# Kernel optimization log

Measured on AMD Instinct MI355X. Metric: run time of the kernel, lower is better.

## Reference

```python
import jax, jax.numpy as jnp
import numpy as np

BATCH, SEQ, HEADS, EMB = 16, 4096, 16, 64
SHAPE = int(SEQ ** 0.5)          # 64 (2D grid side)
N = 2 * SHAPE - 1                # 127 (circular conv length)


def setup_inputs() -> dict:
    key = jax.random.key(0)
    k_v, k_w = jax.random.split(key)
    v = jax.random.normal(k_v, (BATCH, SEQ, HEADS, EMB), dtype=jnp.float32)
    # 'full' bias base: learned relative bias of length 2*shape_-1 per head
    w = jax.random.normal(k_w, (1, HEADS, N), dtype=jnp.float32)
    o_ = jnp.ones((SHAPE,), dtype=jnp.float32)
    return {"v": v, "w": w, "o_": o_}


def reference(v, w, o_):
    B, S, H, E = v.shape
    s = int(S ** 0.5)
    n = 2 * s - 1

    # bias_base_type == 'full': slice w[..., shape_-s : shape_+s-1] == all of w
    z_fft = jnp.fft.rfft(w)                              # (1, H, n//2+1) complex

    # v: [B, S, H, E] -> [B, E, H, s1, s2]
    vt = jnp.transpose(v, (0, 3, 2, 1)).reshape(B, E, H, s, s)
    v_s = vt.sum(axis=3)                                 # sum over s1 -> [B, E, H, s2]
    u_s = vt.sum(axis=4)                                 # sum over s2 -> [B, E, H, s1]

    pad = ((0, 0), (0, 0), (0, 0), (s - 1, 0))
    v_m_fft = jnp.fft.rfft(jnp.pad(v_s, pad))            # [B, E, H, n//2+1]
    u_m_fft = jnp.fft.rfft(jnp.pad(u_s, pad))

    zf = z_fft[:, None]                                  # (1, 1, H, n//2+1)
    RxV = jnp.fft.irfft(v_m_fft * zf, n=n)[..., :s]      # [B, E, H, s]
    RxU = jnp.fft.irfft(u_m_fft * zf, n=n)[..., :s]      # [B, E, H, s]

    # outer sum over the 2D grid, flatten back to seq
    pbv = RxV[..., None, :] + RxU[..., :, None]          # [B, E, H, s, s]
    pbv = pbv.reshape(B, E, H, S)
    pbv = jnp.transpose(pbv, (0, 3, 2, 1))               # [B, S, H, E]

    # normalizer term z_pb (batch independent)
    o_pad = jnp.pad(o_, ((s - 1, 0),))                   # (n,)
    o_fft = jnp.fft.rfft(o_pad)                          # (n//2+1,)
    z_pb = jnp.fft.irfft(o_fft * z_fft, n=n)[..., :s] * s  # (1, H, s)
    z_pb = z_pb[..., None, :] + z_pb[..., :, None]       # (1, H, s, s)
    z_pb = z_pb.reshape(-1, H, s * s)                    # (1, H, S)
    z_pb = jnp.transpose(z_pb, (0, 2, 1))                # (1, S, H)

    return pbv, z_pb
```

## Files before the change

### kernel.cpp

```cpp
#include <hip/hip_runtime.h>

#define BATCH 16
#define SEQ   4096
#define HEADS 16
#define EMB   64
#define SS    64
#define NW    127

#define RX_ELEMS (BATCH * SS * HEADS * EMB)

__global__ __launch_bounds__(256, 4) void reduce_conv_kernel(
    const float* __restrict__ v, const float* __restrict__ w,
    float* __restrict__ rxv, float* __restrict__ rxu)
{
    __shared__ float vsf[SS][SS];
    __shared__ float usl[16][SS];
    __shared__ float wtab[NW];

    const int blk  = blockIdx.x;
    const int c    = blk & 3;
    const int bh   = blk >> 2;
    const int b    = bh >> 4;
    const int h    = bh & (HEADS - 1);
    const int tid  = threadIdx.x;
    const int wave = tid >> 6;
    const int lane = tid & 63;

    for (int idx = tid; idx < SS * SS; idx += 256) (&vsf[0][0])[idx] = 0.0f;
    if (tid < NW) wtab[tid] = w[h * NW + tid];
    __syncthreads();

    const float* vbase = v + ((size_t)b * SEQ * HEADS + h) * EMB + lane;
    float vsacc[SS];
    #pragma unroll
    for (int j = 0; j < SS; ++j) vsacc[j] = 0.0f;

    const int r0 = wave * 4;
    for (int rr = 0; rr < 4; ++rr) {
        const int i = c * 16 + r0 + rr;
        const float* rowp = vbase + (size_t)i * SS * (HEADS * EMB);
        float uacc = 0.0f;
        #pragma unroll
        for (int j = 0; j < SS; ++j) {
            const float val = rowp[(size_t)j * (HEADS * EMB)];
            uacc += val;
            vsacc[j] += val;
        }
        usl[r0 + rr][lane] = uacc;
    }
    #pragma unroll
    for (int j = 0; j < SS; ++j) atomicAdd(&vsf[j][lane], vsacc[j]);
    __syncthreads();

    const int t0 = wave * 16;
    float accv[16], accu[16];
    #pragma unroll
    for (int tt = 0; tt < 16; ++tt) { accv[tt] = 0.0f; accu[tt] = 0.0f; }

    #pragma unroll
    for (int jb = 0; jb < 4; ++jb) {
        float wreg[31];
        #pragma unroll
        for (int d = 0; d < 31; ++d) {
            int idx = t0 - jb * 16 + 49 + d;
            if (idx >= NW) idx -= NW;
            wreg[d] = wtab[idx];
        }
        #pragma unroll
        for (int jj = 0; jj < 16; ++jj) {
            const float cv = vsf[jb * 16 + jj][lane];
            #pragma unroll
            for (int tt = 0; tt < 16; ++tt)
                accv[tt] += wreg[15 + tt - jj] * cv;
        }
    }
    {
        float wreg[31];
        #pragma unroll
        for (int d = 0; d < 31; ++d) {
            int idx = t0 - c * 16 + 49 + d;
            if (idx >= NW) idx -= NW;
            wreg[d] = wtab[idx];
        }
        #pragma unroll
        for (int rr = 0; rr < 16; ++rr) {
            const float cu = usl[rr][lane];
            #pragma unroll
            for (int tt = 0; tt < 16; ++tt)
                accu[tt] += wreg[15 + tt - rr] * cu;
        }
    }

    const size_t base = (((size_t)b * SS) << 10) + (h << 6) + lane;
    #pragma unroll
    for (int tt = 0; tt < 16; ++tt) {
        const size_t o = base + ((size_t)(t0 + tt) << 10);
        atomicAdd(&rxv[o], accv[tt]);
        atomicAdd(&rxu[o], accu[tt]);
    }
}

__global__ __launch_bounds__(256) void expand_kernel(
    const float* __restrict__ rxv, const float* __restrict__ rxu,
    float* __restrict__ out)
{
    const int blk = blockIdx.x;
    const int b   = blk >> 6;
    const int tid = threadIdx.x;

    const float4 ru = *((const float4*)(rxu + ((size_t)blk << 10)) + tid);
    const float4* rvb = (const float4*)(rxv + ((size_t)b << 16));
    float4* ob = (float4*)(out + (((size_t)blk) << 16)) + tid;

    #pragma unroll 8
    for (int j = 0; j < SS; ++j) {
        float4 rv = rvb[(j << 8) + tid];
        float4 r;
        r.x = rv.x + ru.x; r.y = rv.y + ru.y;
        r.z = rv.z + ru.z; r.w = rv.w + ru.w;
        ob[(size_t)j << 8] = r;
    }
}

__global__ __launch_bounds__(256) void zpb_kernel(const float* __restrict__ w,
                                                  const float* __restrict__ o_,
                                                  float* __restrict__ out2) {
    __shared__ float zp[HEADS][SS];
    __shared__ float osh[SS];
    __shared__ float wsh[HEADS * NW];

    const int tid = threadIdx.x;
    const int g   = blockIdx.x;

    if (tid < SS) osh[tid] = o_[tid];
    for (int idx = tid; idx < HEADS * NW; idx += 256) wsh[idx] = w[idx];
    __syncthreads();

    for (int idx = tid; idx < HEADS * SS; idx += 256) {
        const int h = idx / SS, t = idx % SS;
        float acc = 0.0f;
        #pragma unroll
        for (int j = 0; j < SS; ++j) {
            int k = t - j + 64;
            if (k >= NW) k -= NW;
            acc += osh[j] * wsh[h * NW + k];
        }
        zp[h][t] = acc * (float)SS;
    }
    __syncthreads();

    for (int idx = tid; idx < SS * HEADS; idx += 256) {
        const int tl = idx / HEADS, h = idx % HEADS;
        out2[(size_t)(g * SS + tl) * HEADS + h] = zp[h][tl] + zp[h][g];
    }
}

extern "C" void kernel_launch(void* const* d_in, const int* in_sizes, int n_in,
                              void* d_out, int out_size, void* d_ws, size_t ws_size,
                              hipStream_t stream) {
    const float* v  = (const float*)d_in[0];
    const float* w  = (const float*)d_in[1];
    const float* o_ = (const float*)d_in[2];
    float* out = (float*)d_out;

    float* rxv = (float*)d_ws;
    float* rxu = rxv + RX_ELEMS;

    hipMemsetAsync(d_ws, 0, (size_t)2 * RX_ELEMS * sizeof(float), stream);

    reduce_conv_kernel<<<BATCH * HEADS * 4, 256, 0, stream>>>(v, w, rxv, rxu);
    expand_kernel<<<BATCH * SS, 256, 0, stream>>>(rxv, rxu, out);

    const size_t out1_elems = (size_t)BATCH * SEQ * HEADS * EMB;
    zpb_kernel<<<SS, 256, 0, stream>>>(w, o_, out + out1_elems);
}
```

Baseline: 567.2 us.

## Split reduction and convolution into separate kernels with vectorized coalesced sums

Replaces the fused reduce+conv kernel with a sums kernel that streams v using float4 loads over the full contiguous head×emb plane (1024-thread blocks) and writes row and column sums to workspace. A second conv kernel then runs one block per (batch, head), doing both convolutions in one pass and storing with plain writes instead of atomics. The intent is better memory coalescing and bandwidth on the dominant read of v, at the cost of an extra kernel launch, an extra workspace round trip, and global atomics for the column sums.

```diff
diff --git a/kernel.cpp b/kernel.cpp
--- a/kernel.cpp
+++ b/kernel.cpp
@@ -6,50 +6,90 @@
 #define EMB   64
 #define SS    64
 #define NW    127
-
-#define RX_ELEMS (BATCH * SS * HEADS * EMB)
-
-__global__ __launch_bounds__(256, 4) void reduce_conv_kernel(
-    const float* __restrict__ v, const float* __restrict__ w,
-    float* __restrict__ rxv, float* __restrict__ rxu)
+#define PLANE (HEADS * EMB)
+
+#define SUMS_ELEMS (BATCH * SS * PLANE)
+
+__global__ __launch_bounds__(1024) void sums_kernel(
+    const float4* __restrict__ v4, float* __restrict__ vs,
+    float4* __restrict__ us4)
 {
-    __shared__ float vsf[SS][SS];
-    __shared__ float usl[16][SS];
+    __shared__ float4 upart[4][4][256];
+
+    const int blk = blockIdx.x;
+    const int b   = blk >> 4;
+    const int ic  = blk & 15;
+    const int tid = threadIdx.x;
+    const int g   = tid >> 8;
+    const int t   = tid & 255;
+
+    const float4* base = v4 + ((size_t)(b * SEQ + ic * 256) << 8) + t;
+
+    float4 uacc[4], vacc[16];
+    #pragma unroll
+    for (int il = 0; il < 4; ++il) uacc[il] = make_float4(0.f, 0.f, 0.f, 0.f);
+    #pragma unroll
+    for (int jj = 0; jj < 16; ++jj) vacc[jj] = make_float4(0.f, 0.f, 0.f, 0.f);
+
+    #pragma unroll
+    for (int il = 0; il < 4; ++il) {
+        const float4* p = base + ((size_t)(il * 64 + g * 16) << 8);
+        #pragma unroll
+        for (int jj = 0; jj < 16; ++jj) {
+            const float4 x = p[(size_t)jj << 8];
+            uacc[il].x += x.x; uacc[il].y += x.y; uacc[il].z += x.z; uacc[il].w += x.w;
+            vacc[jj].x += x.x; vacc[jj].y += x.y; vacc[jj].z += x.z; vacc[jj].w += x.w;
+        }
+    }
+
+    #pragma unroll
+    for (int il = 0; il < 4; ++il) upart[g][il][t] = uacc[il];
+    __syncthreads();
+    {
+        const int il2 = tid >> 8;
+        float4 s = upart[0][il2][t];
+        #pragma unroll
+        for (int gg = 1; gg < 4; ++gg) {
+            const float4 q = upart[gg][il2][t];
+            s.x += q.x; s.y += q.y; s.z += q.z; s.w += q.w;
+        }
+        us4[((size_t)(b * SS + ic * 4 + il2) << 8) + t] = s;
+    }
+
+    float* vsp = vs + ((size_t)(b * SS + g * 16) << 10) + (t << 2);
+    #pragma unroll
+    for (int jj = 0; jj < 16; ++jj) {
+        float* p = vsp + ((size_t)jj << 10);
+        atomicAdd(p + 0, vacc[jj].x);
+        atomicAdd(p + 1, vacc[jj].y);
+        atomicAdd(p + 2, vacc[jj].z);
+        atomicAdd(p + 3, vacc[jj].w);
+    }
+}
+
+__global__ __launch_bounds__(256) void conv_kernel(
+    const float* __restrict__ w, const float* __restrict__ vs,
+    const float* __restrict__ us, float* __restrict__ rxv,
+    float* __restrict__ rxu)
+{
     __shared__ float wtab[NW];
-
-    const int blk  = blockIdx.x;
-    const int c    = blk & 3;
-    const int bh   = blk >> 2;
+    __shared__ float vsl[SS][SS];
+    __shared__ float usl[SS][SS];
+
+    const int bh   = blockIdx.x;
     const int b    = bh >> 4;
     const int h    = bh & (HEADS - 1);
     const int tid  = threadIdx.x;
     const int wave = tid >> 6;
     const int lane = tid & 63;
 
-    for (int idx = tid; idx < SS * SS; idx += 256) (&vsf[0][0])[idx] = 0.0f;
     if (tid < NW) wtab[tid] = w[h * NW + tid];
-    __syncthreads();
-
-    const float* vbase = v + ((size_t)b * SEQ * HEADS + h) * EMB + lane;
-    float vsacc[SS];
-    #pragma unroll
-    for (int j = 0; j < SS; ++j) vsacc[j] = 0.0f;
-
-    const int r0 = wave * 4;
-    for (int rr = 0; rr < 4; ++rr) {
-        const int i = c * 16 + r0 + rr;
-        const float* rowp = vbase + (size_t)i * SS * (HEADS * EMB);
-        float uacc = 0.0f;
-        #pragma unroll
-        for (int j = 0; j < SS; ++j) {
-            const float val = rowp[(size_t)j * (HEADS * EMB)];
-            uacc += val;
-            vsacc[j] += val;
-        }
-        usl[r0 + rr][lane] = uacc;
-    }
-    #pragma unroll
-    for (int j = 0; j < SS; ++j) atomicAdd(&vsf[j][lane], vsacc[j]);
+    for (int idx = tid; idx < SS * SS; idx += 256) {
+        const int j = idx >> 6, e = idx & 63;
+        const size_t gofs = ((size_t)(b * SS + j) << 10) + (h << 6) + e;
+        vsl[j][e] = vs[gofs];
+        usl[j][e] = us[gofs];
+    }
     __syncthreads();
 
     const int t0 = wave * 16;
@@ -68,35 +108,22 @@
         }
         #pragma unroll
         for (int jj = 0; jj < 16; ++jj) {
-            const float cv = vsf[jb * 16 + jj][lane];
+            const float cv = vsl[jb * 16 + jj][lane];
+            const float cu = usl[jb * 16 + jj][lane];
             #pragma unroll
-            for (int tt = 0; tt < 16; ++tt)
-                accv[tt] += wreg[15 + tt - jj] * cv;
-        }
-    }
-    {
-        float wreg[31];
-        #pragma unroll
-        for (int d = 0; d < 31; ++d) {
-            int idx = t0 - c * 16 + 49 + d;
-            if (idx >= NW) idx -= NW;
-            wreg[d] = wtab[idx];
-        }
-        #pragma unroll
-        for (int rr = 0; rr < 16; ++rr) {
-            const float cu = usl[rr][lane];
-            #pragma unroll
-            for (int tt = 0; tt < 16; ++tt)
-                accu[tt] += wreg[15 + tt - rr] * cu;
-        }
-    }
-
-    const size_t base = (((size_t)b * SS) << 10) + (h << 6) + lane;
+            for (int tt = 0; tt < 16; ++tt) {
+                const float cw = wreg[15 + tt - jj];
+                accv[tt] += cw * cv;
+                accu[tt] += cw * cu;
+            }
+        }
+    }
+
     #pragma unroll
     for (int tt = 0; tt < 16; ++tt) {
-        const size_t o = base + ((size_t)(t0 + tt) << 10);
-        atomicAdd(&rxv[o], accv[tt]);
-        atomicAdd(&rxu[o], accu[tt]);
+        const size_t o = ((size_t)(b * SS + t0 + tt) << 10) + (h << 6) + lane;
+        rxv[o] = accv[tt];
+        rxu[o] = accu[tt];
     }
 }
 
@@ -163,12 +190,15 @@
     const float* o_ = (const float*)d_in[2];
     float* out = (float*)d_out;
 
-    float* rxv = (float*)d_ws;
-    float* rxu = rxv + RX_ELEMS;
-
-    hipMemsetAsync(d_ws, 0, (size_t)2 * RX_ELEMS * sizeof(float), stream);
-
-    reduce_conv_kernel<<<BATCH * HEADS * 4, 256, 0, stream>>>(v, w, rxv, rxu);
+    float* vs  = (float*)d_ws;
+    float* us  = vs  + SUMS_ELEMS;
+    float* rxv = us  + SUMS_ELEMS;
+    float* rxu = rxv + SUMS_ELEMS;
+
+    hipMemsetAsync(vs, 0, (size_t)SUMS_ELEMS * sizeof(float), stream);
+
+    sums_kernel<<<BATCH * 16, 1024, 0, stream>>>((const float4*)v, vs, (float4*)us);
+    conv_kernel<<<BATCH * HEADS, 256, 0, stream>>>(w, vs, us, rxv, rxu);
     expand_kernel<<<BATCH * SS, 256, 0, stream>>>(rxv, rxu, out);
 
     const size_t out1_elems = (size_t)BATCH * SEQ * HEADS * EMB;
```

New measurement: 671.0 us. 1.18x slower.
